# Performance work log

Hardware: AMD Instinct MI355X
Metric: run time of the kernel (lower is better)

## Reference

```python
import jax, jax.numpy as jnp
import numpy as np

N_NODES = 100000
K_HOPS = 3  # PyG TAGConv default


def _gcn_norm(edge_index, num_nodes):
    # Symmetric normalization WITHOUT self-loops (TAGConv default).
    row, col = edge_index[0], edge_index[1]
    ones = jnp.ones(row.shape[0], dtype=jnp.float32)
    deg = jax.ops.segment_sum(ones, col, num_segments=num_nodes)
    dinv = jnp.where(deg > 0, jax.lax.rsqrt(jnp.maximum(deg, 1.0)), 0.0)
    return dinv[row] * dinv[col]


def _tagconv(x, row, col, norm, W, b, num_nodes):
    # out = Linear(concat_{k=0..K} (D^-1/2 A D^-1/2)^k x)
    xs = [x]
    h = x
    for _ in range(K_HOPS):
        h = jax.ops.segment_sum(norm[:, None] * h[row], col, num_segments=num_nodes)
        xs.append(h)
    return jnp.concatenate(xs, axis=-1) @ W.T + b


def setup_inputs() -> dict:
    key = jax.random.key(0)
    k1, k2, k3, k4, k5 = jax.random.split(key, 5)
    in_c, hid_c, out_c = 128, 128, 128
    n_edges = 1600000
    x = jax.random.normal(k1, (N_NODES, in_c), dtype=jnp.float32)
    edge_index = jax.random.randint(k2, (2, n_edges), 0, N_NODES, dtype=jnp.int64)
    s1 = 1.0 / np.sqrt(in_c * (K_HOPS + 1))
    s2 = 1.0 / np.sqrt(hid_c * (K_HOPS + 1))
    W1 = jax.random.normal(k3, (hid_c, in_c * (K_HOPS + 1)), dtype=jnp.float32) * s1
    b1 = jnp.zeros((hid_c,), dtype=jnp.float32)
    W2 = jax.random.normal(k4, (out_c, hid_c * (K_HOPS + 1)), dtype=jnp.float32) * s2
    b2 = jnp.zeros((out_c,), dtype=jnp.float32)
    return {"x": x, "edge_index": edge_index, "W1": W1, "b1": b1, "W2": W2, "b2": b2}


def reference(x, edge_index, W1, b1, W2, b2):
    row, col = edge_index[0], edge_index[1]
    norm = _gcn_norm(edge_index, N_NODES)  # [E]
    h = jax.nn.relu(_tagconv(x, row, col, norm, W1, b1, N_NODES))
    out = _tagconv(h, row, col, norm, W2, b2, N_NODES)
    return out.reshape(-1)  # original: x.view(n_nodes * out_channels)
```

## Files before the change

kernel.cpp:

```cpp
#include <hip/hip_runtime.h>
#include <hip/hip_fp16.h>

#define FEAT 128
#define BSH 8
#define BSZ 256
#define NBMAX 400
#define ABLK 4096
#define CAP 6144

typedef _Float16 half_t;
typedef _Float16 half4 __attribute__((ext_vector_type(4)));
typedef _Float16 half8 __attribute__((ext_vector_type(8)));
typedef float float4v __attribute__((ext_vector_type(4)));

__global__ void binit_kernel(int* __restrict__ gcur, int NB) {
    int b = blockIdx.x * blockDim.x + threadIdx.x;
    if (b < NB) gcur[b * 16] = b * CAP;
}

__global__ __launch_bounds__(256) void bucketA_kernel(const int* __restrict__ row,
                                                      const int* __restrict__ col,
                                                      int* __restrict__ gcur,
                                                      long long* __restrict__ tmp,
                                                      int E, int NB) {
    __shared__ int hist[NBMAX];
    __shared__ int gbase[NBMAX];
    int t = threadIdx.x;
    int base = blockIdx.x * ABLK;
    for (int i = t; i < NB; i += 256) hist[i] = 0;
    __syncthreads();
    int r[16], c[16];
#pragma unroll
    for (int j = 0; j < 16; ++j) {
        int e = base + j * 256 + t;
        if (e < E) {
            r[j] = __builtin_nontemporal_load(row + e);
            c[j] = __builtin_nontemporal_load(col + e);
            atomicAdd(&hist[c[j] >> BSH], 1);
        } else c[j] = -1;
    }
    __syncthreads();
    for (int b = t; b < NB; b += 256) {
        int cnt = hist[b];
        if (cnt > 0) gbase[b] = atomicAdd(&gcur[b * 16], cnt);
    }
    __syncthreads();
    for (int i = t; i < NB; i += 256) hist[i] = 0;
    __syncthreads();
#pragma unroll
    for (int j = 0; j < 16; ++j) {
        if (c[j] >= 0) {
            int b = c[j] >> BSH;
            int lpos = atomicAdd(&hist[b], 1);
            long long pk = ((long long)(unsigned)c[j] << 32) | (unsigned)r[j];
            tmp[gbase[b] + lpos] = pk;
        }
    }
}

__global__ __launch_bounds__(512) void bscan_kernel(const int* __restrict__ gcur,
                                                    int* __restrict__ bbase,
                                                    int* __restrict__ offsN, int NB) {
    __shared__ int sd[512];
    int t = threadIdx.x;
    int v = (t < NB) ? (gcur[t * 16] - t * CAP) : 0;
    sd[t] = v;
    __syncthreads();
    for (int o = 1; o < 512; o <<= 1) {
        int u = (t >= o) ? sd[t - o] : 0;
        __syncthreads();
        sd[t] += u;
        __syncthreads();
    }
    if (t < NB) bbase[t] = sd[t] - v;
    if (t == NB - 1) *offsN = sd[t];
}

__global__ __launch_bounds__(256) void bdeg_kernel(const long long* __restrict__ tmp,
                                                   const int* __restrict__ gcur,
                                                   const int* __restrict__ bbase,
                                                   int* __restrict__ offs,
                                                   float* __restrict__ dinv, int N) {
    __shared__ int ldeg[BSZ];
    __shared__ int sums[BSZ];
    int b = blockIdx.x;
    int lo = b << BSH;
    int t = threadIdx.x;
    int cnt = gcur[b * 16] - b * CAP;
    ldeg[t] = 0;
    __syncthreads();
    const long long* reg = tmp + (size_t)b * CAP;
    for (int i = t; i < cnt; i += 256) {
        int c = (int)(__builtin_nontemporal_load(reg + i) >> 32);
        atomicAdd(&ldeg[c - lo], 1);
    }
    __syncthreads();
    int d = ldeg[t];
    sums[t] = d;
    __syncthreads();
    for (int o = 1; o < 256; o <<= 1) {
        int u = (t >= o) ? sums[t - o] : 0;
        __syncthreads();
        sums[t] += u;
        __syncthreads();
    }
    int node = lo + t;
    if (node < N) {
        offs[node] = bbase[b] + sums[t] - d;
        dinv[node] = (d > 0) ? rsqrtf((float)d) : 0.0f;
    }
}

__global__ __launch_bounds__(256) void bplace_kernel(const long long* __restrict__ tmp,
                                                     const int* __restrict__ gcur,
                                                     const int* __restrict__ offs,
                                                     int* __restrict__ csr, int N) {
    __shared__ int lcur[BSZ];
    int b = blockIdx.x;
    int lo = b << BSH;
    int hi = lo + BSZ;
    if (hi > N) hi = N;
    int t = threadIdx.x;
    int cnt = gcur[b * 16] - b * CAP;
    if (t < hi - lo) lcur[t] = offs[lo + t];
    __syncthreads();
    const long long* reg = tmp + (size_t)b * CAP;
    for (int i = t; i < cnt; i += 256) {
        long long pk = __builtin_nontemporal_load(reg + i);
        int r = (int)(pk & 0xffffffffLL);
        int c = (int)(pk >> 32);
        int pos = atomicAdd(&lcur[c - lo], 1);
        csr[pos] = r;
    }
}

__global__ void zrow_kernel(half_t* a, half_t* b, half_t* c, half_t* d, half_t* e, int N) {
    int t = threadIdx.x;
    size_t o = (size_t)N * FEAT + t;
    a[o] = (half_t)0.0f; b[o] = (half_t)0.0f; c[o] = (half_t)0.0f;
    d[o] = (half_t)0.0f; e[o] = (half_t)0.0f;
}

__global__ void f2h3_kernel(const float* __restrict__ a, half_t* __restrict__ ah,
                            half_t* __restrict__ gh, const float* __restrict__ dinv, int na4,
                            const float* __restrict__ b, half_t* __restrict__ bh, int nb4,
                            const float* __restrict__ c, half_t* __restrict__ ch, int nc4) {
    int i = blockIdx.x * blockDim.x + threadIdx.x;
    int j = i;
    if (j < na4) {
        float4 v = ((const float4*)a)[j];
        half4 o;
        o.x = (half_t)v.x; o.y = (half_t)v.y; o.z = (half_t)v.z; o.w = (half_t)v.w;
        ((half4*)ah)[j] = o;
        float dv = dinv[j >> 5];
        half4 g;
        g.x = (half_t)(v.x * dv); g.y = (half_t)(v.y * dv);
        g.z = (half_t)(v.z * dv); g.w = (half_t)(v.w * dv);
        ((half4*)gh)[j] = g;
        return;
    }
    j -= na4;
    const float* src;
    half_t* dst;
    if (j < nb4) { src = b; dst = bh; }
    else if ((j -= nb4) < nc4) { src = c; dst = ch; }
    else return;
    float4 v = ((const float4*)src)[j];
    half4 o;
    o.x = (half_t)v.x; o.y = (half_t)v.y; o.z = (half_t)v.z; o.w = (half_t)v.w;
    ((half4*)dst)[j] = o;
}

__global__ __launch_bounds__(256) void prop16_kernel(const half_t* __restrict__ src,
                                                     half_t* __restrict__ dst,
                                                     const int* __restrict__ offs,
                                                     const int* __restrict__ csr,
                                                     const float* __restrict__ dinv, int N) {
    int v = blockIdx.x * 4 + (threadIdx.x >> 6);
    if (v >= N) return;
    int lane = threadIdx.x & 63;
    int q = lane >> 4;
    int p = lane & 15;
    int s0 = offs[v];
    int s1 = offs[v + 1];
    int last = s1 - 1;
    half8 accA = (half8)(half_t)0.0f;
    half8 accB = (half8)(half_t)0.0f;
    for (int base = s0; base < s1; base += 32) {
        int rr[8];
#pragma unroll
        for (int k = 0; k < 8; ++k) {
            int i = base + k * 4 + q;
            int ic = (i < s1) ? i : last;
            int r = __builtin_nontemporal_load(csr + ic);
            rr[k] = (i < s1) ? r : N;
        }
        half8 g0 = *(const half8*)(src + (size_t)rr[0] * FEAT + p * 8);
        half8 g1 = *(const half8*)(src + (size_t)rr[1] * FEAT + p * 8);
        half8 g2 = *(const half8*)(src + (size_t)rr[2] * FEAT + p * 8);
        half8 g3 = *(const half8*)(src + (size_t)rr[3] * FEAT + p * 8);
        half8 g4 = *(const half8*)(src + (size_t)rr[4] * FEAT + p * 8);
        half8 g5 = *(const half8*)(src + (size_t)rr[5] * FEAT + p * 8);
        half8 g6 = *(const half8*)(src + (size_t)rr[6] * FEAT + p * 8);
        half8 g7 = *(const half8*)(src + (size_t)rr[7] * FEAT + p * 8);
        accA = accA + g0; accB = accB + g1;
        accA = accA + g2; accB = accB + g3;
        accA = accA + g4; accB = accB + g5;
        accA = accA + g6; accB = accB + g7;
    }
    half8 acc = accA + accB;
    union U { half8 h; int i[4]; };
    U u, o1;
    u.h = acc;
#pragma unroll
    for (int k = 0; k < 4; ++k) o1.i[k] = __shfl_xor(u.i[k], 32, 64);
    u.h = u.h + o1.h;
#pragma unroll
    for (int k = 0; k < 4; ++k) o1.i[k] = __shfl_xor(u.i[k], 16, 64);
    u.h = u.h + o1.h;
    if (lane < 16) {
        float d = dinv[v];
        float d2 = d * d;
        half8 outv;
#pragma unroll
        for (int j = 0; j < 8; ++j) outv[j] = (half_t)((float)u.h[j] * d2);
        *(half8*)(dst + (size_t)v * FEAT + p * 8) = outv;
    }
}

template <bool RELU, bool HALFOUT>
__global__ __launch_bounds__(256) void gemm16_kernel(const half_t* __restrict__ H0,
                                                     const half_t* __restrict__ H1,
                                                     const half_t* __restrict__ H2,
                                                     const half_t* __restrict__ H3,
                                                     const half_t* __restrict__ W,
                                                     const float* __restrict__ bias,
                                                     const float* __restrict__ dinv,
                                                     half_t* __restrict__ out_h,
                                                     half_t* __restrict__ gout,
                                                     float* __restrict__ out_f, int N) {
    __shared__ half_t ws[4][128][40];
    const int tid = threadIdx.x;
    const int lane = tid & 63;
    const int wid = tid >> 6;
    const int lr = lane & 15;
    const int lk = lane >> 4;
    const int m = blockIdx.x * 64 + wid * 16 + lr;
    const bool mok = (m < N);

    float dm = mok ? dinv[m] : 0.0f;
    half_t hs = (half_t)((dm > 0.0f) ? 1.0f / dm : 0.0f);

    float4v acc[8];
#pragma unroll
    for (int ct = 0; ct < 8; ++ct) acc[ct] = (float4v)0.0f;

    const half_t* Hs[4] = {H0, H1, H2, H3};
    const int wo = tid >> 1;
    const int wh = tid & 1;

#pragma unroll
    for (int b = 0; b < 4; ++b) {
        const half_t* __restrict__ H = Hs[b];
        half8 hf[4];
#pragma unroll
        for (int kt = 0; kt < 4; ++kt) {
            hf[kt] = (half8)(half_t)0.0f;
            if (mok) hf[kt] = *(const half8*)(H + (size_t)m * FEAT + kt * 32 + lk * 8);
            if (b > 0) hf[kt] = hf[kt] * hs;
        }
        const half8* wsrc = (const half8*)(W + (size_t)wo * 512 + b * 128 + wh * 64);
        half8 wv[8];
#pragma unroll
        for (int j = 0; j < 8; ++j) wv[j] = wsrc[j];
        __syncthreads();
#pragma unroll
        for (int j = 0; j < 8; ++j) {
            int kt = wh * 2 + (j >> 2);
            int ko = (j & 3) * 8;
            *(half8*)&ws[kt][wo][ko] = wv[j];
        }
        __syncthreads();
#pragma unroll
        for (int kt = 0; kt < 4; ++kt) {
#pragma unroll
            for (int ct = 0; ct < 8; ++ct) {
                half8 wfrag = *(const half8*)&ws[kt][ct * 16 + lr][lk * 8];
                acc[ct] = __builtin_amdgcn_mfma_f32_16x16x32_f16(wfrag, hf[kt], acc[ct], 0, 0, 0);
            }
        }
    }

    if (mok) {
        half_t hd = (half_t)dm;
#pragma unroll
        for (int ct = 0; ct < 8; ++ct) {
            int o = ct * 16 + lk * 4;
            float4 bv = *(const float4*)(bias + o);
            float r0 = acc[ct][0] + bv.x;
            float r1 = acc[ct][1] + bv.y;
            float r2 = acc[ct][2] + bv.z;
            float r3 = acc[ct][3] + bv.w;
            if (RELU) {
                r0 = fmaxf(r0, 0.0f); r1 = fmaxf(r1, 0.0f);
                r2 = fmaxf(r2, 0.0f); r3 = fmaxf(r3, 0.0f);
            }
            if (HALFOUT) {
                half4 hv;
                hv.x = (half_t)r0; hv.y = (half_t)r1; hv.z = (half_t)r2; hv.w = (half_t)r3;
                *(half4*)(out_h + (size_t)m * FEAT + o) = hv;
                half4 gv = hv * hd;
                *(half4*)(gout + (size_t)m * FEAT + o) = gv;
            } else {
                float4 fv;
                fv.x = r0; fv.y = r1; fv.z = r2; fv.w = r3;
                *(float4*)(out_f + (size_t)m * FEAT + o) = fv;
            }
        }
    }
}

extern "C" void kernel_launch(void* const* d_in, const int* in_sizes, int n_in,
                              void* d_out, int out_size, void* d_ws, size_t ws_size,
                              hipStream_t stream) {
    const float* x   = (const float*)d_in[0];
    const int*   ei  = (const int*)d_in[1];
    const float* W1  = (const float*)d_in[2];
    const float* b1  = (const float*)d_in[3];
    const float* W2  = (const float*)d_in[4];
    const float* b2  = (const float*)d_in[5];
    float* out = (float*)d_out;

    const int N = in_sizes[0] / FEAT;
    const int E = in_sizes[1] / 2;
    const int* row = ei;
    const int* col = ei + E;
    const int NB = (N + BSZ - 1) / BSZ;

    size_t off = 0;
    auto carve = [&](size_t bytes) -> void* {
        void* p = (char*)d_ws + off;
        off += (bytes + 255) & ~(size_t)255;
        return p;
    };
    float*     dinv  = (float*)carve((size_t)N * 4);
    int*       offs  = (int*)carve((size_t)(N + 1) * 4);
    int*       bbase = (int*)carve((size_t)NB * 4);
    int*       gcur  = (int*)carve((size_t)NB * 16 * 4);
    long long* tmp   = (long long*)carve((size_t)NB * CAP * 8);
    int*       csr   = (int*)carve((size_t)(E + 64) * 4);
    half_t*    x16   = (half_t*)carve((size_t)N * FEAT * 2);
    half_t*    g0    = (half_t*)carve((size_t)(N + 1) * FEAT * 2);
    half_t*    t1    = (half_t*)carve((size_t)(N + 1) * FEAT * 2);
    half_t*    t2    = (half_t*)carve((size_t)(N + 1) * FEAT * 2);
    half_t*    t3    = (half_t*)carve((size_t)(N + 1) * FEAT * 2);
    half_t*    hbuf  = (half_t*)carve((size_t)N * FEAT * 2);
    half_t*    ghbuf = (half_t*)carve((size_t)(N + 1) * FEAT * 2);
    half_t*    w1h   = (half_t*)carve((size_t)FEAT * 512 * 2);
    half_t*    w2h   = (half_t*)carve((size_t)FEAT * 512 * 2);

    const int tB = 256;
    const int gA = (E + ABLK - 1) / ABLK;
    const int gP = (N + 3) / 4;
    const int gG = (N + 63) / 64;
    const int xt4 = N * FEAT / 4;
    const int wt4 = FEAT * 512 / 4;
    const int cvt_total = xt4 + 2 * wt4;

    binit_kernel<<<(NB + tB - 1) / tB, tB, 0, stream>>>(gcur, NB);
    bucketA_kernel<<<gA, 256, 0, stream>>>(row, col, gcur, tmp, E, NB);
    bscan_kernel<<<1, 512, 0, stream>>>(gcur, bbase, offs + N, NB);
    bdeg_kernel<<<NB, 256, 0, stream>>>(tmp, gcur, bbase, offs, dinv, N);
    bplace_kernel<<<NB, 256, 0, stream>>>(tmp, gcur, offs, csr, N);

    zrow_kernel<<<1, 128, 0, stream>>>(g0, t1, t2, t3, ghbuf, N);
    f2h3_kernel<<<(cvt_total + tB - 1) / tB, tB, 0, stream>>>(x, x16, g0, dinv, xt4,
                                                              W1, w1h, wt4, W2, w2h, wt4);

    prop16_kernel<<<gP, 256, 0, stream>>>(g0, t1, offs, csr, dinv, N);
    prop16_kernel<<<gP, 256, 0, stream>>>(t1, t2, offs, csr, dinv, N);
    prop16_kernel<<<gP, 256, 0, stream>>>(t2, t3, offs, csr, dinv, N);
    gemm16_kernel<true, true><<<gG, 256, 0, stream>>>(x16, t1, t2, t3, w1h, b1, dinv,
                                                      hbuf, ghbuf, nullptr, N);

    prop16_kernel<<<gP, 256, 0, stream>>>(ghbuf, t1, offs, csr, dinv, N);
    prop16_kernel<<<gP, 256, 0, stream>>>(t1, t2, offs, csr, dinv, N);
    prop16_kernel<<<gP, 256, 0, stream>>>(t2, t3, offs, csr, dinv, N);
    gemm16_kernel<false, false><<<gG, 256, 0, stream>>>(hbuf, t1, t2, t3, w2h, b2, dinv,
                                                        nullptr, nullptr, out, N);
}
```

Measured before the change: 517.6 us.

## Read GEMM weights directly from global memory and compute two row tiles per wave

```diff
diff --git a/kernel.cpp b/kernel.cpp
--- a/kernel.cpp
+++ b/kernel.cpp
@@ -239,59 +239,58 @@
                                                      half_t* __restrict__ out_h,
                                                      half_t* __restrict__ gout,
                                                      float* __restrict__ out_f, int N) {
-    __shared__ half_t ws[4][128][40];
     const int tid = threadIdx.x;
     const int lane = tid & 63;
     const int wid = tid >> 6;
     const int lr = lane & 15;
     const int lk = lane >> 4;
-    const int m = blockIdx.x * 64 + wid * 16 + lr;
-    const bool mok = (m < N);
-
-    float dm = mok ? dinv[m] : 0.0f;
-    half_t hs = (half_t)((dm > 0.0f) ? 1.0f / dm : 0.0f);
-
-    float4v acc[8];
-#pragma unroll
-    for (int ct = 0; ct < 8; ++ct) acc[ct] = (float4v)0.0f;
+    const int mb = blockIdx.x * 128 + wid * 32;
+    const int m0 = mb + lr;
+    const int m1 = mb + 16 + lr;
+    const bool ok0 = (m0 < N);
+    const bool ok1 = (m1 < N);
+
+    const float dm0 = ok0 ? dinv[m0] : 0.0f;
+    const float dm1 = ok1 ? dinv[m1] : 0.0f;
+    const half_t hs0 = (half_t)((dm0 > 0.0f) ? 1.0f / dm0 : 0.0f);
+    const half_t hs1 = (half_t)((dm1 > 0.0f) ? 1.0f / dm1 : 0.0f);
+
+    float4v acc0[8], acc1[8];
+#pragma unroll
+    for (int ct = 0; ct < 8; ++ct) { acc0[ct] = (float4v)0.0f; acc1[ct] = (float4v)0.0f; }
 
     const half_t* Hs[4] = {H0, H1, H2, H3};
-    const int wo = tid >> 1;
-    const int wh = tid & 1;
 
 #pragma unroll
     for (int b = 0; b < 4; ++b) {
         const half_t* __restrict__ H = Hs[b];
-        half8 hf[4];
+        half8 hf0[4], hf1[4];
 #pragma unroll
         for (int kt = 0; kt < 4; ++kt) {
-            hf[kt] = (half8)(half_t)0.0f;
-            if (mok) hf[kt] = *(const half8*)(H + (size_t)m * FEAT + kt * 32 + lk * 8);
-            if (b > 0) hf[kt] = hf[kt] * hs;
-        }
-        const half8* wsrc = (const half8*)(W + (size_t)wo * 512 + b * 128 + wh * 64);
-        half8 wv[8];
-#pragma unroll
-        for (int j = 0; j < 8; ++j) wv[j] = wsrc[j];
-        __syncthreads();
-#pragma unroll
-        for (int j = 0; j < 8; ++j) {
-            int kt = wh * 2 + (j >> 2);
-            int ko = (j & 3) * 8;
-            *(half8*)&ws[kt][wo][ko] = wv[j];
-        }
-        __syncthreads();
+            hf0[kt] = (half8)(half_t)0.0f;
+            hf1[kt] = (half8)(half_t)0.0f;
+            if (ok0) hf0[kt] = *(const half8*)(H + (size_t)m0 * FEAT + kt * 32 + lk * 8);
+            if (ok1) hf1[kt] = *(const half8*)(H + (size_t)m1 * FEAT + kt * 32 + lk * 8);
+            if (b > 0) { hf0[kt] = hf0[kt] * hs0; hf1[kt] = hf1[kt] * hs1; }
+        }
 #pragma unroll
         for (int kt = 0; kt < 4; ++kt) {
 #pragma unroll
             for (int ct = 0; ct < 8; ++ct) {
-                half8 wfrag = *(const half8*)&ws[kt][ct * 16 + lr][lk * 8];
-                acc[ct] = __builtin_amdgcn_mfma_f32_16x16x32_f16(wfrag, hf[kt], acc[ct], 0, 0, 0);
+                half8 wf = *(const half8*)(W + (size_t)(ct * 16 + lr) * 512 + b * 128 + kt * 32 + lk * 8);
+                acc0[ct] = __builtin_amdgcn_mfma_f32_16x16x32_f16(wf, hf0[kt], acc0[ct], 0, 0, 0);
+                acc1[ct] = __builtin_amdgcn_mfma_f32_16x16x32_f16(wf, hf1[kt], acc1[ct], 0, 0, 0);
             }
         }
     }
 
-    if (mok) {
+#pragma unroll
+    for (int tile = 0; tile < 2; ++tile) {
+        int m = tile ? m1 : m0;
+        bool ok = tile ? ok1 : ok0;
+        float dm = tile ? dm1 : dm0;
+        float4v* acc = tile ? acc1 : acc0;
+        if (!ok) continue;
         half_t hd = (half_t)dm;
 #pragma unroll
         for (int ct = 0; ct < 8; ++ct) {
@@ -362,7 +361,7 @@
     const int tB = 256;
     const int gA = (E + ABLK - 1) / ABLK;
     const int gP = (N + 3) / 4;
-    const int gG = (N + 63) / 64;
+    const int gG = (N + 127) / 128;
     const int xt4 = N * FEAT / 4;
     const int wt4 = FEAT * 512 / 4;
     const int cvt_total = xt4 + 2 * wt4;
```

Measured after the change: 582.3 us. +12.5%, slower.
